# Optimization experiments

Measured on AMD Instinct MI355X. Metric: run time of the kernel, lower is better.

## Reference

```python
import jax, jax.numpy as jnp
import numpy as np

B, C, N = 2, 1024, 80
D = 3 * C + 2  # 3074 token dim
DFF = 2048     # torch TransformerEncoderLayer default dim_feedforward
HW = 224
REFINE = 3
EPS = 1e-5


def _layernorm(x, g, b):
    m = jnp.mean(x, axis=-1, keepdims=True)
    v = jnp.mean((x - m) ** 2, axis=-1, keepdims=True)
    return g * (x - m) / jnp.sqrt(v + EPS) + b


def _pos_encoding(seq_len, dim):
    pos = jnp.arange(seq_len, dtype=jnp.float32)[:, None]
    div = jnp.exp(jnp.arange(0, dim, 2, dtype=jnp.float32) * (-np.log(10000.0) / dim))
    pe = jnp.zeros((seq_len, dim), dtype=jnp.float32)
    pe = pe.at[:, 0::2].set(jnp.sin(pos * div)).at[:, 1::2].set(jnp.cos(pos * div))
    return pe


def _forward(pre_f, curr_f, first_f, ln_g, ln_b, ipw, ipb, opw, opb,
             n1g, n1b, l1w, l1b, l2w, l2b, n2g, n2b, ow, ob,
             prev_b, first_b):
    # --- vectorized find_best_shift: batched circular L1 correlation ---
    idx = (jnp.arange(N)[None, :] - jnp.arange(N)[:, None]) % N  # [shift, pos]
    rolled = first_b[:, idx]                                     # [B, N, N, 2]
    dist = jnp.abs(prev_b[:, None] - rolled).sum(axis=(-1, -2))  # [B, N]
    best = jnp.argmin(dist, axis=1)                              # first min, like torch loop
    roll_idx = (jnp.arange(N)[None, :] - best[:, None]) % N      # [B, N]
    first_b = jax.vmap(lambda fb, ri: fb[ri])(first_b, roll_idx)

    # --- bilinear upsample to 224x224 (F.interpolate, align_corners=False) ---
    up = lambda f: jax.image.resize(f, (f.shape[0], f.shape[1], HW, HW), method='bilinear')
    pre_up, curr_up, first_up = up(pre_f), up(curr_f), up(first_f)

    # --- vectorized get_bou_features: [B,N,C] gather ---
    gather = jax.vmap(lambda f, b: f[:, b[:, 0], b[:, 1]].T)
    pre_q = gather(pre_up, prev_b)      # [B, N, C]
    first_q = gather(first_up, first_b)  # [B, N, C]

    pe = _pos_encoding(N, D)
    curr = prev_b.astype(jnp.float32)
    scale = 1.0 / jnp.sqrt(jnp.float32(D))
    results = []
    for _ in range(REFINE):
        bf = gather(curr_up, curr.astype(jnp.int32))          # [B, N, C]
        tokens = jnp.concatenate([pre_q, bf, curr, first_q], axis=-1)  # [B, N, D]
        tokens = _layernorm(tokens, ln_g, ln_b)
        tokens = tokens + pe[None]
        # --- TransformerEncoderLayer (post-norm, nhead=1, relu, eval/no dropout) ---
        qkv = tokens @ ipw.T + ipb
        q, k, v = jnp.split(qkv, 3, axis=-1)
        attn = jax.nn.softmax(jnp.einsum('bqd,bkd->bqk', q, k) * scale, axis=-1)
        a = jnp.einsum('bqk,bkd->bqd', attn, v) @ opw.T + opb
        x = _layernorm(tokens + a, n1g, n1b)
        ff = jax.nn.relu(x @ l1w.T + l1b) @ l2w.T + l2b
        x = _layernorm(x + ff, n2g, n2b)
        out = x @ ow.T + ob                                   # [B, N, 1026]
        curr = jnp.clip(curr + out[..., C:], 0.0, 223.0)
        pre_q = pre_q + out[..., :C]
        results.append(curr)
    return jnp.stack(results)  # [REFINE, B, N, 2]


def setup_inputs() -> dict:
    key = jax.random.key(0)
    ks = jax.random.split(key, 12)
    f = lambda i, s: jax.random.normal(ks[i], s, dtype=jnp.float32)
    w = lambda i, s: 0.02 * jax.random.normal(ks[i], s, dtype=jnp.float32)
    return {
        'pre_img_features': f(0, (B, C, 14, 14)),
        'curr_img_features': f(1, (B, C, 14, 14)),
        'first_img_features': f(2, (B, C, 14, 14)),
        'previous_boundary': jax.random.randint(ks[3], (B, N, 2), 0, HW),
        'first_boundary': jax.random.randint(ks[4], (B, N, 2), 0, HW),
        'ln_g': jnp.ones((D,), jnp.float32), 'ln_b': jnp.zeros((D,), jnp.float32),
        'in_proj_w': w(5, (3 * D, D)), 'in_proj_b': jnp.zeros((3 * D,), jnp.float32),
        'out_proj_w': w(6, (D, D)), 'out_proj_b': jnp.zeros((D,), jnp.float32),
        'norm1_g': jnp.ones((D,), jnp.float32), 'norm1_b': jnp.zeros((D,), jnp.float32),
        'lin1_w': w(7, (DFF, D)), 'lin1_b': jnp.zeros((DFF,), jnp.float32),
        'lin2_w': w(8, (D, DFF)), 'lin2_b': jnp.zeros((D,), jnp.float32),
        'norm2_g': jnp.ones((D,), jnp.float32), 'norm2_b': jnp.zeros((D,), jnp.float32),
        'out_w': w(9, (C + 2, D)), 'out_b': jnp.zeros((C + 2,), jnp.float32),
    }


def reference(pre_img_features, curr_img_features, first_img_features,
              previous_boundary, first_boundary,
              ln_g, ln_b, in_proj_w, in_proj_b, out_proj_w, out_proj_b,
              norm1_g, norm1_b, lin1_w, lin1_b, lin2_w, lin2_b,
              norm2_g, norm2_b, out_w, out_b):
    return _forward(pre_img_features, curr_img_features, first_img_features,
                    ln_g, ln_b, in_proj_w, in_proj_b, out_proj_w, out_proj_b,
                    norm1_g, norm1_b, lin1_w, lin1_b, lin2_w, lin2_b,
                    norm2_g, norm2_b, out_w, out_b,
                    previous_boundary, first_boundary)
```

## Files before the change

kernel.cpp:

```cpp
#include <hip/hip_runtime.h>
#include <math.h>

#define B_    2
#define C_    1024
#define N_    80
#define D_    3074
#define DFF_  2048
#define OD_   1026
#define QKV_  9222
#define M_    160
#define EPS_  1e-5f
#define KPD_  3104

#define SQKV 6
#define SOP  14
#define SFF1 14
#define SFF2 16
#define SHD  14

typedef __attribute__((ext_vector_type(8))) short bf16x8;
typedef __attribute__((ext_vector_type(4))) float f32x4;

__device__ inline short f2bf(float f) {
    unsigned u = __float_as_uint(f);
    u += 0x7fffu + ((u >> 16) & 1u);
    return (short)(u >> 16);
}

__device__ inline float wave_sum(float v) {
#pragma unroll
    for (int off = 32; off > 0; off >>= 1) v += __shfl_down(v, off, 64);
    return v;
}

__device__ inline float wave_max(float v) {
#pragma unroll
    for (int off = 32; off > 0; off >>= 1) v = fmaxf(v, __shfl_down(v, off, 64));
    return v;
}

__device__ inline void block_reduce_2(float& s, float& s2, float* red) {
    int tid = threadIdx.x;
    int lane = tid & 63, wid = tid >> 6;
    s = wave_sum(s);
    s2 = wave_sum(s2);
    if (lane == 0) { red[wid] = s; red[4 + wid] = s2; }
    __syncthreads();
    if (tid == 0) {
        red[8] = red[0] + red[1] + red[2] + red[3];
        red[9] = red[4] + red[5] + red[6] + red[7];
    }
    __syncthreads();
    s = red[8]; s2 = red[9];
}

__device__ inline void bilin_setup(int p, int& i0, int& i1, float& t) {
    float s = (p + 0.5f) * 0.0625f - 0.5f;
    s = fminf(fmaxf(s, 0.0f), 13.0f);
    i0 = (int)s;
    t = s - (float)i0;
    i1 = min(i0 + 1, 13);
}

__device__ inline float bilin_tap(const float* f, int y0, int y1, float ty,
                                  int x0, int x1, float tx) {
    float a = f[y0 * 14 + x0], b = f[y0 * 14 + x1];
    float c = f[y1 * 14 + x0], d = f[y1 * 14 + x1];
    return (1.f - ty) * ((1.f - tx) * a + tx * b) + ty * ((1.f - tx) * c + tx * d);
}

__global__ __launch_bounds__(128) void align_kernel(const int* __restrict__ prev_b,
                                                    const int* __restrict__ first_b,
                                                    int* __restrict__ fb_al) {
    int b = blockIdx.x;
    int tid = threadIdx.x;
    __shared__ int dist[N_];
    __shared__ int bestIdx;
    if (tid < N_) {
        int s = 0;
        for (int j = 0; j < N_; ++j) {
            int src = (j - tid) % N_;
            if (src < 0) src += N_;
            int dy = prev_b[(b * N_ + j) * 2] - first_b[(b * N_ + src) * 2];
            int dx = prev_b[(b * N_ + j) * 2 + 1] - first_b[(b * N_ + src) * 2 + 1];
            s += abs(dy) + abs(dx);
        }
        dist[tid] = s;
    }
    __syncthreads();
    if (tid == 0) {
        int best = 0, bd = dist[0];
        for (int i = 1; i < N_; ++i)
            if (dist[i] < bd) { bd = dist[i]; best = i; }
        bestIdx = best;
    }
    __syncthreads();
    if (tid < N_) {
        int src = (tid - bestIdx) % N_;
        if (src < 0) src += N_;
        fb_al[(b * N_ + tid) * 2]     = first_b[(b * N_ + src) * 2];
        fb_al[(b * N_ + tid) * 2 + 1] = first_b[(b * N_ + src) * 2 + 1];
    }
}

__global__ __launch_bounds__(256) void gather_init_kernel(
        const float* __restrict__ pre_f, const float* __restrict__ first_f,
        const int* __restrict__ prev_b, const int* __restrict__ fb_al,
        float* __restrict__ pre_q, float* __restrict__ first_q,
        float* __restrict__ curr) {
    int m = blockIdx.x;
    int b = m / N_;
    int tid = threadIdx.x;
    int py = prev_b[m * 2], px = prev_b[m * 2 + 1];
    int fy = fb_al[m * 2], fx = fb_al[m * 2 + 1];
    int py0, py1, px0, px1, fy0, fy1, fx0, fx1;
    float pty, ptx, fty, ftx;
    bilin_setup(py, py0, py1, pty);
    bilin_setup(px, px0, px1, ptx);
    bilin_setup(fy, fy0, fy1, fty);
    bilin_setup(fx, fx0, fx1, ftx);
    for (int c = tid; c < C_; c += 256) {
        const float* fp = pre_f + (size_t)(b * C_ + c) * 196;
        const float* ff = first_f + (size_t)(b * C_ + c) * 196;
        pre_q[(size_t)m * C_ + c]   = bilin_tap(fp, py0, py1, pty, px0, px1, ptx);
        first_q[(size_t)m * C_ + c] = bilin_tap(ff, fy0, fy1, fty, fx0, fx1, ftx);
    }
    if (tid < 2) curr[m * 2 + tid] = (float)prev_b[m * 2 + tid];
}

__global__ __launch_bounds__(256) void tokens_kernel(
        const float* __restrict__ curr_f, const float* __restrict__ pre_q,
        const float* __restrict__ first_q, const float* __restrict__ curr,
        const float* __restrict__ ln_g, const float* __restrict__ ln_b,
        float* __restrict__ tokens, short* __restrict__ tokens_bf) {
    int m = blockIdx.x;
    int b = m / N_;
    int n = m % N_;
    int tid = threadIdx.x;
    __shared__ float bf[C_];
    __shared__ float red[10];

    float cy = curr[m * 2], cx = curr[m * 2 + 1];
    int iy = (int)cy, ix = (int)cx;
    int y0, y1, x0, x1;
    float ty, tx;
    bilin_setup(iy, y0, y1, ty);
    bilin_setup(ix, x0, x1, tx);
    for (int c = tid; c < C_; c += 256) {
        const float* f = curr_f + (size_t)(b * C_ + c) * 196;
        bf[c] = bilin_tap(f, y0, y1, ty, x0, x1, tx);
    }
    __syncthreads();

    float s = 0.f, s2 = 0.f;
    for (int d = tid; d < D_; d += 256) {
        float v;
        if (d < C_)            v = pre_q[(size_t)m * C_ + d];
        else if (d < 2 * C_)   v = bf[d - C_];
        else if (d == 2 * C_)  v = cy;
        else if (d == 2*C_+1)  v = cx;
        else                   v = first_q[(size_t)m * C_ + (d - 2 * C_ - 2)];
        s += v; s2 += v * v;
    }
    block_reduce_2(s, s2, red);
    float mean = s / (float)D_;
    float var = s2 / (float)D_ - mean * mean;
    float inv = rsqrtf(var + EPS_);

    const float negLogDivD = -logf(10000.0f) / (float)D_;
    for (int d = tid; d < KPD_; d += 256) {
        if (d < D_) {
            float v;
            if (d < C_)            v = pre_q[(size_t)m * C_ + d];
            else if (d < 2 * C_)   v = bf[d - C_];
            else if (d == 2 * C_)  v = cy;
            else if (d == 2*C_+1)  v = cx;
            else                   v = first_q[(size_t)m * C_ + (d - 2 * C_ - 2)];
            float ln = ln_g[d] * (v - mean) * inv + ln_b[d];
            int kk = d >> 1;
            float ang = (float)n * expf((float)(2 * kk) * negLogDivD);
            float pe = (d & 1) ? cosf(ang) : sinf(ang);
            float val = ln + pe;
            tokens[(size_t)m * D_ + d] = val;
            tokens_bf[(size_t)m * KPD_ + d] = f2bf(val);
        } else {
            tokens_bf[(size_t)m * KPD_ + d] = 0;
        }
    }
}

__global__ __launch_bounds__(256) void wpack_kernel(const float* __restrict__ w,
                                                    short* __restrict__ o,
                                                    int K, int O, int nch) {
    int s = blockIdx.x;
    int items = nch * 64;
    int qlen = (items + 3) >> 2;
    int beg = blockIdx.y * qlen;
    int end = min(items, beg + qlen);
    for (int idx = beg + threadIdx.x; idx < end; idx += 256) {
        int c = idx >> 6, l = idx & 63;
        int col = l & 15, quad = l >> 4;
        int orow = s * 16 + col;
        int k0 = c * 32 + quad * 8;
        bf16x8 v;
        if (orow < O && k0 + 8 <= K) {
            const float* src = w + (size_t)orow * K + k0;
            float2 a = *(const float2*)(src);
            float2 b = *(const float2*)(src + 2);
            float2 cc = *(const float2*)(src + 4);
            float2 d = *(const float2*)(src + 6);
            v[0] = f2bf(a.x);  v[1] = f2bf(a.y);
            v[2] = f2bf(b.x);  v[3] = f2bf(b.y);
            v[4] = f2bf(cc.x); v[5] = f2bf(cc.y);
            v[6] = f2bf(d.x);  v[7] = f2bf(d.y);
        } else {
#pragma unroll
            for (int j = 0; j < 8; ++j) {
                int k = k0 + j;
                v[j] = (orow < O && k < K) ? f2bf(w[(size_t)orow * K + k]) : (short)0;
            }
        }
        *(bf16x8*)(o + ((size_t)s * nch + c) * 512 + l * 8) = v;
    }
}

template <int SW>
__global__ __launch_bounds__(256) void gemm_stage(
        const short* __restrict__ A, const short* __restrict__ Wp,
        const float* __restrict__ bias, float* __restrict__ part,
        int KpA, int nch, int O, int per) {
    int cs = blockIdx.y * per;
    int ce = min(nch, cs + per);
    if (cs >= ce) return;
    int tid = threadIdx.x;
    int lane = tid & 63, wave = tid >> 6;
    int col = lane & 15, quad = lane >> 4;
    int s0 = (blockIdx.x * 4 + wave) * SW;

    __shared__ short lbuf[2][160 * 32];

    int m0 = tid >> 2, p8 = (tid & 3) * 8;
    int m1 = (tid + 256) >> 2;
    int m2 = (tid + 512) >> 2;
    const short* a0 = A + (size_t)m0 * KpA + p8;
    const short* a1 = A + (size_t)m1 * KpA + p8;
    const short* a2 = A + (size_t)m2 * KpA + p8;
    bf16x8 sr0, sr1, sr2;

    f32x4 acc[SW][10];
#pragma unroll
    for (int j = 0; j < SW; ++j)
#pragma unroll
        for (int t = 0; t < 10; ++t)
#pragma unroll
            for (int r = 0; r < 4; ++r) acc[j][t][r] = 0.f;

    const short* wbase[SW];
#pragma unroll
    for (int j = 0; j < SW; ++j)
        wbase[j] = Wp + (size_t)(s0 + j) * nch * 512 + lane * 8;
    bf16x8 wc[SW], wn[SW];

    sr0 = *(const bf16x8*)(a0 + cs * 32);
    sr1 = *(const bf16x8*)(a1 + cs * 32);
    if (tid < 128) sr2 = *(const bf16x8*)(a2 + cs * 32);
#pragma unroll
    for (int j = 0; j < SW; ++j)
        wc[j] = *(const bf16x8*)(wbase[j] + (size_t)cs * 512);
    *(bf16x8*)(&lbuf[0][m0 * 32 + p8]) = sr0;
    *(bf16x8*)(&lbuf[0][m1 * 32 + p8]) = sr1;
    if (tid < 128) *(bf16x8*)(&lbuf[0][m2 * 32 + p8]) = sr2;
    __syncthreads();

    int cur = 0;
    for (int c = cs; c < ce; ++c) {
        bool more = (c + 1) < ce;
        if (more) {
            sr0 = *(const bf16x8*)(a0 + (c + 1) * 32);
            sr1 = *(const bf16x8*)(a1 + (c + 1) * 32);
            if (tid < 128) sr2 = *(const bf16x8*)(a2 + (c + 1) * 32);
#pragma unroll
            for (int j = 0; j < SW; ++j)
                wn[j] = *(const bf16x8*)(wbase[j] + (size_t)(c + 1) * 512);
        }
#pragma unroll
        for (int t = 0; t < 10; ++t) {
            bf16x8 af = *(const bf16x8*)(&lbuf[cur][t * 512 + col * 32 + quad * 8]);
#pragma unroll
            for (int j = 0; j < SW; ++j)
                acc[j][t] = __builtin_amdgcn_mfma_f32_16x16x32_bf16(af, wc[j], acc[j][t], 0, 0, 0);
        }
        if (more) {
            *(bf16x8*)(&lbuf[cur ^ 1][m0 * 32 + p8]) = sr0;
            *(bf16x8*)(&lbuf[cur ^ 1][m1 * 32 + p8]) = sr1;
            if (tid < 128) *(bf16x8*)(&lbuf[cur ^ 1][m2 * 32 + p8]) = sr2;
        }
        __syncthreads();
#pragma unroll
        for (int j = 0; j < SW; ++j) wc[j] = wn[j];
        cur ^= 1;
    }

    float* pout = part + (size_t)blockIdx.y * M_ * O;
#pragma unroll
    for (int j = 0; j < SW; ++j) {
        int oc = (s0 + j) * 16 + col;
        if (oc < O) {
            float bv = (blockIdx.y == 0) ? bias[oc] : 0.f;
#pragma unroll
            for (int t = 0; t < 10; ++t)
#pragma unroll
                for (int r = 0; r < 4; ++r)
                    pout[(size_t)(t * 16 + quad * 4 + r) * O + oc] = acc[j][t][r] + bv;
        }
    }
}

__global__ __launch_bounds__(256) void gemm_pk(
        const short* __restrict__ A, const short* __restrict__ Wp,
        const float* __restrict__ bias, float* __restrict__ Cout,
        int KpA, int nch, int O) {
    int strip = blockIdx.x;
    int nsk = gridDim.y;
    int mg = blockIdx.z;
    int lane = threadIdx.x & 63, wave = threadIdx.x >> 6;
    int col = lane & 15, quad = lane >> 4;

    int per = (nch + nsk - 1) / nsk;
    int cs = blockIdx.y * per;
    int ce = min(nch, cs + per);
    if (cs >= ce) return;
    int tot = ce - cs;
    int qn = tot >> 2, rmd = tot & 3;
    int c0 = cs + wave * qn + min(wave, rmd);
    int c1 = c0 + qn + (wave < rmd ? 1 : 0);

    const short* wp = Wp + (size_t)strip * nch * 512 + lane * 8;
    const short* ap = A + (size_t)(mg * 80 + col) * KpA + quad * 8;

    f32x4 acc[5];
#pragma unroll
    for (int t = 0; t < 5; ++t)
#pragma unroll
        for (int r = 0; r < 4; ++r) acc[t][r] = 0.f;

    if (c0 < c1) {
        bf16x8 wcur = *(const bf16x8*)(wp + (size_t)c0 * 512);
        for (int c = c0; c < c1; ++c) {
            bf16x8 wnxt = wcur;
            if (c + 1 < c1) wnxt = *(const bf16x8*)(wp + (size_t)(c + 1) * 512);
#pragma unroll
            for (int t = 0; t < 5; ++t) {
                bf16x8 af = *(const bf16x8*)(ap + (size_t)t * 16 * KpA + c * 32);
                acc[t] = __builtin_amdgcn_mfma_f32_16x16x32_bf16(af, wcur, acc[t], 0, 0, 0);
            }
            wcur = wnxt;
        }
    }

    __shared__ f32x4 red[4][5][64];
#pragma unroll
    for (int t = 0; t < 5; ++t) red[wave][t][lane] = acc[t];
    __syncthreads();
    for (int item = threadIdx.x; item < 320; item += 256) {
        int t = item >> 6, l2 = item & 63;
        f32x4 v = red[0][t][l2];
#pragma unroll
        for (int w = 1; w < 4; ++w)
#pragma unroll
            for (int r = 0; r < 4; ++r) v[r] += red[w][t][l2][r];
        int oc = strip * 16 + (l2 & 15);
        if (oc < O) {
            float bv = (blockIdx.y == 0) ? bias[oc] : 0.f;
            int rbase = mg * 80 + t * 16 + (l2 >> 4) * 4;
#pragma unroll
            for (int r = 0; r < 4; ++r) {
                float val = v[r] + bv;
                if (nsk == 1) Cout[(size_t)(rbase + r) * O + oc] = val;
                else atomicAdd(&Cout[(size_t)(rbase + r) * O + oc], val);
            }
        }
    }
}

__global__ __launch_bounds__(256) void gemm_mfma_sk(
        const short* __restrict__ A, const float* __restrict__ Wf,
        const float* __restrict__ bias, float* __restrict__ Cout,
        int K, int KpA, int O, int KC) {
    int kc0 = blockIdx.y * KC;
    if (kc0 >= K) return;
    int kend = min(K, kc0 + KC);

    int lane = threadIdx.x & 63;
    int wave = threadIdx.x >> 6;
    int col  = lane & 15;
    int quad = lane >> 4;
    int o0 = blockIdx.x * 128 + wave * 32 + col;
    int o1 = o0 + 16;
    int oc0 = min(o0, O - 1), oc1 = min(o1, O - 1);

    const float* wrow0 = Wf + (size_t)oc0 * K + quad * 8;
    const float* wrow1 = Wf + (size_t)oc1 * K + quad * 8;
    const short* abase = A + (size_t)col * KpA + quad * 8;

    f32x4 acc0[10], acc1[10];
#pragma unroll
    for (int t = 0; t < 10; ++t)
#pragma unroll
        for (int r = 0; r < 4; ++r) { acc0[t][r] = 0.f; acc1[t][r] = 0.f; }

    int nfull = (kend - kc0) >> 5;
    bf16x8 aCur[10];
    float2 wCur[8];
    if (nfull > 0) {
#pragma unroll
        for (int t = 0; t < 10; ++t)
            aCur[t] = *(const bf16x8*)(abase + (size_t)t * 16 * KpA + kc0);
#pragma unroll
        for (int j = 0; j < 4; ++j) {
            wCur[j]     = *(const float2*)(wrow0 + kc0 + 2 * j);
            wCur[4 + j] = *(const float2*)(wrow1 + kc0 + 2 * j);
        }
    }
    for (int i = 0; i < nfull; ++i) {
        bf16x8 aNxt[10];
        float2 wNxt[8];
        if (i + 1 < nfull) {
            int kn = kc0 + (i + 1) * 32;
#pragma unroll
            for (int t = 0; t < 10; ++t)
                aNxt[t] = *(const bf16x8*)(abase + (size_t)t * 16 * KpA + kn);
#pragma unroll
            for (int j = 0; j < 4; ++j) {
                wNxt[j]     = *(const float2*)(wrow0 + kn + 2 * j);
                wNxt[4 + j] = *(const float2*)(wrow1 + kn + 2 * j);
            }
        }
        bf16x8 b0, b1;
#pragma unroll
        for (int j = 0; j < 4; ++j) {
            b0[2*j] = f2bf(wCur[j].x);     b0[2*j+1] = f2bf(wCur[j].y);
            b1[2*j] = f2bf(wCur[4+j].x);   b1[2*j+1] = f2bf(wCur[4+j].y);
        }
#pragma unroll
        for (int t = 0; t < 10; ++t) {
            acc0[t] = __builtin_amdgcn_mfma_f32_16x16x32_bf16(aCur[t], b0, acc0[t], 0, 0, 0);
            acc1[t] = __builtin_amdgcn_mfma_f32_16x16x32_bf16(aCur[t], b1, acc1[t], 0, 0, 0);
        }
#pragma unroll
        for (int t = 0; t < 10; ++t) aCur[t] = aNxt[t];
#pragma unroll
        for (int j = 0; j < 8; ++j) wCur[j] = wNxt[j];
    }
    int kmain = kc0 + nfull * 32;
    if (kmain < kend) {
        bf16x8 b0, b1;
#pragma unroll
        for (int j = 0; j < 8; ++j) {
            int k = kmain + quad * 8 + j;
            b0[j] = (k < kend) ? f2bf(Wf[(size_t)oc0 * K + k]) : (short)0;
            b1[j] = (k < kend) ? f2bf(Wf[(size_t)oc1 * K + k]) : (short)0;
        }
#pragma unroll
        for (int t = 0; t < 10; ++t) {
            bf16x8 af = *(const bf16x8*)(abase + (size_t)t * 16 * KpA + kmain);
            acc0[t] = __builtin_amdgcn_mfma_f32_16x16x32_bf16(af, b0, acc0[t], 0, 0, 0);
            acc1[t] = __builtin_amdgcn_mfma_f32_16x16x32_bf16(af, b1, acc1[t], 0, 0, 0);
        }
    }
    if (o0 < O) {
        float bv = (blockIdx.y == 0) ? bias[o0] : 0.f;
#pragma unroll
        for (int t = 0; t < 10; ++t)
#pragma unroll
            for (int r = 0; r < 4; ++r)
                atomicAdd(&Cout[(size_t)(t * 16 + quad * 4 + r) * O + o0], acc0[t][r] + bv);
    }
    if (o1 < O) {
        float bv = (blockIdx.y == 0) ? bias[o1] : 0.f;
#pragma unroll
        for (int t = 0; t < 10; ++t)
#pragma unroll
            for (int r = 0; r < 4; ++r)
                atomicAdd(&Cout[(size_t)(t * 16 + quad * 4 + r) * O + o1], acc1[t][r] + bv);
    }
}

__global__ __launch_bounds__(256) void relu_cvt_kernel(const float* __restrict__ in,
                                                       int S, size_t sstr,
                                                       short* __restrict__ out,
                                                       int n) {
    int i = blockIdx.x * 256 + threadIdx.x;
    if (i < n) {
        float v = 0.f;
        for (int s = 0; s < S; ++s) v += in[(size_t)s * sstr + i];
        out[i] = f2bf(fmaxf(v, 0.f));
    }
}

__global__ __launch_bounds__(256) void qkv_cvt_kernel(const float* __restrict__ part,
                                                      int S,
                                                      short* __restrict__ q_bf,
                                                      short* __restrict__ k_bf,
                                                      short* __restrict__ v_bf) {
    int m = blockIdx.x;
    int b = m / N_, q = m % N_;
    for (int d = threadIdx.x; d < KPD_; d += 256) {
        short qv = 0, kv = 0, vv = 0;
        if (d < D_) {
            float qf = 0.f, kf = 0.f, vf = 0.f;
            for (int s = 0; s < S; ++s) {
                const float* p = part + (size_t)s * M_ * QKV_ + (size_t)m * QKV_;
                qf += p[d]; kf += p[D_ + d]; vf += p[2 * D_ + d];
            }
            qv = f2bf(qf); kv = f2bf(kf); vv = f2bf(vf);
        }
        q_bf[(size_t)m * KPD_ + d] = qv;
        k_bf[(size_t)m * KPD_ + d] = kv;
        v_bf[((size_t)b * 96 + q) * KPD_ + d] = vv;
    }
}

__global__ __launch_bounds__(256) void scores_mfma(const short* __restrict__ q_bf,
                                                   const short* __restrict__ k_bf,
                                                   float* __restrict__ sc) {
    int bi = blockIdx.x;
    int b = bi / 25, qt = (bi % 25) / 5, kt = bi % 5;
    int lane = threadIdx.x & 63, wave = threadIdx.x >> 6;
    int col = lane & 15, quad = lane >> 4;
    const short* qbase = q_bf + (size_t)(b * N_ + qt * 16 + col) * KPD_ + quad * 8;
    const short* kbase = k_bf + (size_t)(b * N_ + kt * 16 + col) * KPD_ + quad * 8;
    f32x4 acc;
#pragma unroll
    for (int r = 0; r < 4; ++r) acc[r] = 0.f;
    int c0 = wave * 25, c1 = min(97, c0 + 25);
    for (int c = c0; c < c1; ++c) {
        bf16x8 af = *(const bf16x8*)(qbase + c * 32);
        bf16x8 bf8 = *(const bf16x8*)(kbase + c * 32);
        acc = __builtin_amdgcn_mfma_f32_16x16x32_bf16(af, bf8, acc, 0, 0, 0);
    }
    __shared__ f32x4 red[4][64];
    red[wave][lane] = acc;
    __syncthreads();
    if (threadIdx.x < 64) {
        f32x4 t = red[0][lane];
#pragma unroll
        for (int w = 1; w < 4; ++w)
#pragma unroll
            for (int r = 0; r < 4; ++r) t[r] += red[w][lane][r];
        float scale = rsqrtf((float)D_);
#pragma unroll
        for (int r = 0; r < 4; ++r)
            sc[(size_t)(b * N_ + qt * 16 + quad * 4 + r) * N_ + kt * 16 + col] = t[r] * scale;
    }
}

__global__ __launch_bounds__(256) void softmax_kernel(const float* __restrict__ sc,
                                                      short* __restrict__ p_bf) {
    int m = blockIdx.x * 4 + (threadIdx.x >> 6);
    int lane = threadIdx.x & 63;
    const float* row = sc + (size_t)m * N_;
    float a = row[lane];
    float bv = (lane < 16) ? row[64 + lane] : -1e30f;
    float mx = wave_max(fmaxf(a, bv));
    mx = __shfl(mx, 0, 64);
    float e0 = expf(a - mx);
    float e1 = (lane < 16) ? expf(bv - mx) : 0.f;
    float sum = wave_sum(e0 + e1);
    sum = __shfl(sum, 0, 64);
    float rs = 1.0f / sum;
    p_bf[(size_t)m * 96 + lane] = f2bf(e0 * rs);
    if (lane < 32)
        p_bf[(size_t)m * 96 + 64 + lane] = (lane < 16) ? f2bf(e1 * rs) : (short)0;
}

__global__ __launch_bounds__(256) void av_mfma(const short* __restrict__ p_bf,
                                               const short* __restrict__ v_bf,
                                               short* __restrict__ av_bf) {
    int bi = blockIdx.x;
    int b = bi / 49, g = bi % 49;
    int lane = threadIdx.x & 63, wave = threadIdx.x >> 6;
    int dtile = g * 4 + wave;
    if (dtile >= 194) return;
    int d0 = dtile * 16;
    int col = lane & 15, quad = lane >> 4;
    const short* pbase = p_bf + (size_t)b * N_ * 96 + quad * 8;
    const short* vb = v_bf + (size_t)b * 96 * KPD_ + d0 + col;
    f32x4 acc[5];
#pragma unroll
    for (int t = 0; t < 5; ++t)
#pragma unroll
        for (int r = 0; r < 4; ++r) acc[t][r] = 0.f;
#pragma unroll
    for (int c = 0; c < 3; ++c) {
        bf16x8 bf8;
#pragma unroll
        for (int j = 0; j < 8; ++j)
            bf8[j] = vb[(size_t)(c * 32 + quad * 8 + j) * KPD_];
#pragma unroll
        for (int t = 0; t < 5; ++t) {
            bf16x8 af = *(const bf16x8*)(pbase + (size_t)(t * 16 + col) * 96 + c * 32);
            acc[t] = __builtin_amdgcn_mfma_f32_16x16x32_bf16(af, bf8, acc[t], 0, 0, 0);
        }
    }
#pragma unroll
    for (int t = 0; t < 5; ++t)
#pragma unroll
        for (int r = 0; r < 4; ++r)
            av_bf[(size_t)(b * N_ + t * 16 + quad * 4 + r) * KPD_ + d0 + col] = f2bf(acc[t][r]);
}

template <bool WF32>
__global__ __launch_bounds__(256) void ln_kernel(const float* __restrict__ xin,
                                                 int S, size_t sstr,
                                                 const float* __restrict__ res,
                                                 const float* __restrict__ g,
                                                 const float* __restrict__ bta,
                                                 float* __restrict__ outf,
                                                 short* __restrict__ outb) {
    int m = blockIdx.x;
    int tid = threadIdx.x;
    __shared__ float red[10];
    const float* xr = xin + (size_t)m * D_;
    const float* rr = res + (size_t)m * D_;
    float vv[13];
    float s = 0.f, s2 = 0.f;
#pragma unroll
    for (int i = 0; i < 13; ++i) {
        int d = tid + i * 256;
        float v = 0.f;
        if (d < D_) {
            v = rr[d];
            for (int sp = 0; sp < S; ++sp) v += xr[(size_t)sp * sstr + d];
            s += v; s2 += v * v;
        }
        vv[i] = v;
    }
    block_reduce_2(s, s2, red);
    float mean = s / (float)D_;
    float var = s2 / (float)D_ - mean * mean;
    float inv = rsqrtf(var + EPS_);
#pragma unroll
    for (int i = 0; i < 13; ++i) {
        int d = tid + i * 256;
        if (d < D_) {
            float y = g[d] * (vv[i] - mean) * inv + bta[d];
            if (WF32) outf[(size_t)m * D_ + d] = y;
            outb[(size_t)m * KPD_ + d] = f2bf(y);
        } else if (d < KPD_) {
            outb[(size_t)m * KPD_ + d] = 0;
        }
    }
}

__global__ __launch_bounds__(256) void update_kernel(const float* __restrict__ part,
                                                     int S, size_t sstr,
                                                     float* __restrict__ curr,
                                                     float* __restrict__ pre_q,
                                                     float* __restrict__ results) {
    int m = blockIdx.x;
    int tid = threadIdx.x;
    const float* pr = part + (size_t)m * OD_;
    for (int c = tid; c < C_; c += 256) {
        float v = 0.f;
        for (int s = 0; s < S; ++s) v += pr[(size_t)s * sstr + c];
        pre_q[(size_t)m * C_ + c] += v;
    }
    if (tid < 2) {
        float v = 0.f;
        for (int s = 0; s < S; ++s) v += pr[(size_t)s * sstr + C_ + tid];
        float nc = curr[m * 2 + tid] + v;
        nc = fminf(fmaxf(nc, 0.f), 223.f);
        curr[m * 2 + tid] = nc;
        results[m * 2 + tid] = nc;
    }
}

extern "C" void kernel_launch(void* const* d_in, const int* in_sizes, int n_in,
                              void* d_out, int out_size, void* d_ws, size_t ws_size,
                              hipStream_t stream) {
    const float* pre_f   = (const float*)d_in[0];
    const float* curr_f  = (const float*)d_in[1];
    const float* first_f = (const float*)d_in[2];
    const int*   prev_b  = (const int*)d_in[3];
    const int*   first_b = (const int*)d_in[4];
    const float* ln_g    = (const float*)d_in[5];
    const float* ln_b    = (const float*)d_in[6];
    const float* ipw     = (const float*)d_in[7];
    const float* ipb     = (const float*)d_in[8];
    const float* opw     = (const float*)d_in[9];
    const float* opb     = (const float*)d_in[10];
    const float* n1g     = (const float*)d_in[11];
    const float* n1b     = (const float*)d_in[12];
    const float* l1w     = (const float*)d_in[13];
    const float* l1b     = (const float*)d_in[14];
    const float* l2w     = (const float*)d_in[15];
    const float* l2b     = (const float*)d_in[16];
    const float* n2g     = (const float*)d_in[17];
    const float* n2b     = (const float*)d_in[18];
    const float* ow      = (const float*)d_in[19];
    const float* ob      = (const float*)d_in[20];
    float* outp = (float*)d_out;

    float* wf = (float*)d_ws;
    size_t off = 0;
    int*   fb_al   = (int*)(wf + off); off += 320;
    float* curr    = wf + off;         off += 320;
    float* pre_q   = wf + off;         off += (size_t)M_ * C_;
    float* first_q = wf + off;         off += (size_t)M_ * C_;
    float* tokens  = wf + off;         off += (size_t)M_ * D_;
    float* xbuf    = wf + off;         off += (size_t)M_ * D_;
    float* sc      = wf + off;         off += (size_t)M_ * N_;
    short* tokens_bf = (short*)(wf + off); off += (size_t)M_ * KPD_ / 2;
    short* x_bf      = (short*)(wf + off); off += (size_t)M_ * KPD_ / 2;
    short* x2_bf     = (short*)(wf + off); off += (size_t)M_ * KPD_ / 2;
    short* av_bf     = (short*)(wf + off); off += (size_t)M_ * KPD_ / 2;
    short* ff1_bf    = (short*)(wf + off); off += (size_t)M_ * DFF_ / 2;
    short* q_bf      = (short*)(wf + off); off += (size_t)M_ * KPD_ / 2;
    short* k_bf      = (short*)(wf + off); off += (size_t)M_ * KPD_ / 2;
    short* v_bf      = (short*)(wf + off); off += (size_t)B_ * 96 * KPD_ / 2;
    short* p_bf      = (short*)(wf + off); off += (size_t)M_ * 96 / 2;
    size_t commonF = off;

    size_t o2 = commonF;
    short* ipw_p2 = (short*)(wf + o2); o2 += (size_t)584 * 97 * 256;
    short* opw_p2 = (short*)(wf + o2); o2 += (size_t)200 * 97 * 256;
    short* l1w_p2 = (short*)(wf + o2); o2 += (size_t)128 * 97 * 256;
    short* l2w_p2 = (short*)(wf + o2); o2 += (size_t)200 * 64 * 256;
    short* ow_p2  = (short*)(wf + o2); o2 += (size_t)68  * 97 * 256;
    float* gpart  = wf + o2;           o2 += (size_t)SQKV * M_ * QKV_;

    size_t o1 = commonF;
    float* qkv   = wf + o1; o1 += (size_t)M_ * QKV_;
    float* aout  = wf + o1; o1 += (size_t)M_ * D_;
    float* ff1f  = wf + o1; o1 += (size_t)M_ * DFF_;
    float* ffout = wf + o1; o1 += (size_t)M_ * D_;
    float* outb  = wf + o1; o1 += (size_t)M_ * OD_;
    size_t o0 = o1;
    short* ipw_p1 = (short*)(wf + o1); o1 += (size_t)577 * 97 * 256;
    short* opw_p1 = (short*)(wf + o1); o1 += (size_t)193 * 97 * 256;
    short* l1w_p1 = (short*)(wf + o1); o1 += (size_t)128 * 97 * 256;
    short* l2w_p1 = (short*)(wf + o1); o1 += (size_t)193 * 64 * 256;
    short* ow_p1  = (short*)(wf + o1); o1 += (size_t)65  * 97 * 256;

    int tier = (ws_size >= o2 * sizeof(float)) ? 2
             : (ws_size >= o1 * sizeof(float)) ? 1
             : 0;
    (void)in_sizes; (void)n_in; (void)out_size; (void)o0;

    hipLaunchKernelGGL(align_kernel, dim3(B_), dim3(128), 0, stream,
                       prev_b, first_b, fb_al);
    hipLaunchKernelGGL(gather_init_kernel, dim3(M_), dim3(256), 0, stream,
                       pre_f, first_f, prev_b, fb_al, pre_q, first_q, curr);
    hipMemsetAsync(v_bf, 0, (size_t)B_ * 96 * KPD_ * 2, stream);

    if (tier == 2) {
        hipLaunchKernelGGL(wpack_kernel, dim3(584, 4), dim3(256), 0, stream, ipw, ipw_p2, D_, QKV_, 97);
        hipLaunchKernelGGL(wpack_kernel, dim3(200, 4), dim3(256), 0, stream, opw, opw_p2, D_, D_, 97);
        hipLaunchKernelGGL(wpack_kernel, dim3(128, 4), dim3(256), 0, stream, l1w, l1w_p2, D_, DFF_, 97);
        hipLaunchKernelGGL(wpack_kernel, dim3(200, 4), dim3(256), 0, stream, l2w, l2w_p2, DFF_, D_, 64);
        hipLaunchKernelGGL(wpack_kernel, dim3(68, 4),  dim3(256), 0, stream, ow, ow_p2, D_, OD_, 97);
    } else if (tier == 1) {
        hipLaunchKernelGGL(wpack_kernel, dim3(577, 4), dim3(256), 0, stream, ipw, ipw_p1, D_, QKV_, 97);
        hipLaunchKernelGGL(wpack_kernel, dim3(193, 4), dim3(256), 0, stream, opw, opw_p1, D_, D_, 97);
        hipLaunchKernelGGL(wpack_kernel, dim3(128, 4), dim3(256), 0, stream, l1w, l1w_p1, D_, DFF_, 97);
        hipLaunchKernelGGL(wpack_kernel, dim3(193, 4), dim3(256), 0, stream, l2w, l2w_p1, DFF_, D_, 64);
        hipLaunchKernelGGL(wpack_kernel, dim3(65, 4),  dim3(256), 0, stream, ow, ow_p1, D_, OD_, 97);
    }

    for (int it = 0; it < 3; ++it) {
        if (tier < 2) {
            if (tier == 0) hipMemsetAsync(qkv, 0, (size_t)M_ * QKV_ * 4, stream);
            hipMemsetAsync(aout,  0, (size_t)M_ * D_   * 4, stream);
            hipMemsetAsync(ff1f,  0, (size_t)M_ * DFF_ * 4, stream);
            hipMemsetAsync(ffout, 0, (size_t)M_ * D_   * 4, stream);
            hipMemsetAsync(outb,  0, (size_t)M_ * OD_  * 4, stream);
        }

        hipLaunchKernelGGL(tokens_kernel, dim3(M_), dim3(256), 0, stream,
                           curr_f, pre_q, first_q, curr, ln_g, ln_b, tokens, tokens_bf);
        if (tier == 2)
            hipLaunchKernelGGL((gemm_stage<2>), dim3(73, SQKV), dim3(256), 0, stream,
                               tokens_bf, ipw_p2, ipb, gpart, KPD_, 97, QKV_, (97 + SQKV - 1) / SQKV);
        else if (tier == 1)
            hipLaunchKernelGGL(gemm_pk, dim3(577, 1, 2), dim3(256), 0, stream,
                               tokens_bf, ipw_p1, ipb, qkv, KPD_, 97, QKV_);
        else
            hipLaunchKernelGGL(gemm_mfma_sk, dim3(73, 6), dim3(256), 0, stream,
                               tokens_bf, ipw, ipb, qkv, D_, KPD_, QKV_, 544);
        hipLaunchKernelGGL(qkv_cvt_kernel, dim3(M_), dim3(256), 0, stream,
                           (tier == 2) ? gpart : qkv, (tier == 2) ? SQKV : 1,
                           q_bf, k_bf, v_bf);
        hipLaunchKernelGGL(scores_mfma, dim3(50), dim3(256), 0, stream,
                           q_bf, k_bf, sc);
        hipLaunchKernelGGL(softmax_kernel, dim3(40), dim3(256), 0, stream,
                           sc, p_bf);
        hipLaunchKernelGGL(av_mfma, dim3(98), dim3(256), 0, stream,
                           p_bf, v_bf, av_bf);
        if (tier == 2)
            hipLaunchKernelGGL((gemm_stage<2>), dim3(25, SOP), dim3(256), 0, stream,
                               av_bf, opw_p2, opb, gpart, KPD_, 97, D_, (97 + SOP - 1) / SOP);
        else if (tier == 1)
            hipLaunchKernelGGL(gemm_pk, dim3(193, 2, 2), dim3(256), 0, stream,
                               av_bf, opw_p1, opb, aout, KPD_, 97, D_);
        else
            hipLaunchKernelGGL(gemm_mfma_sk, dim3(25, 10), dim3(256), 0, stream,
                               av_bf, opw, opb, aout, D_, KPD_, D_, 320);
        hipLaunchKernelGGL((ln_kernel<true>), dim3(M_), dim3(256), 0, stream,
                           (tier == 2) ? gpart : aout, (tier == 2) ? SOP : 1, (size_t)M_ * D_,
                           tokens, n1g, n1b, xbuf, x_bf);
        if (tier == 2)
            hipLaunchKernelGGL((gemm_stage<2>), dim3(16, SFF1), dim3(256), 0, stream,
                               x_bf, l1w_p2, l1b, gpart, KPD_, 97, DFF_, (97 + SFF1 - 1) / SFF1);
        else if (tier == 1)
            hipLaunchKernelGGL(gemm_pk, dim3(128, 2, 2), dim3(256), 0, stream,
                               x_bf, l1w_p1, l1b, ff1f, KPD_, 97, DFF_);
        else
            hipLaunchKernelGGL(gemm_mfma_sk, dim3(16, 17), dim3(256), 0, stream,
                               x_bf, l1w, l1b, ff1f, D_, KPD_, DFF_, 192);
        hipLaunchKernelGGL(relu_cvt_kernel, dim3((M_ * DFF_ + 255) / 256), dim3(256), 0, stream,
                           (tier == 2) ? gpart : ff1f, (tier == 2) ? SFF1 : 1, (size_t)M_ * DFF_,
                           ff1_bf, M_ * DFF_);
        if (tier == 2)
            hipLaunchKernelGGL((gemm_stage<2>), dim3(25, SFF2), dim3(256), 0, stream,
                               ff1_bf, l2w_p2, l2b, gpart, DFF_, 64, D_, (64 + SFF2 - 1) / SFF2);
        else if (tier == 1)
            hipLaunchKernelGGL(gemm_pk, dim3(193, 2, 2), dim3(256), 0, stream,
                               ff1_bf, l2w_p1, l2b, ffout, DFF_, 64, D_);
        else
            hipLaunchKernelGGL(gemm_mfma_sk, dim3(25, 11), dim3(256), 0, stream,
                               ff1_bf, l2w, l2b, ffout, DFF_, DFF_, D_, 192);
        hipLaunchKernelGGL((ln_kernel<false>), dim3(M_), dim3(256), 0, stream,
                           (tier == 2) ? gpart : ffout, (tier == 2) ? SFF2 : 1, (size_t)M_ * D_,
                           xbuf, n2g, n2b, (float*)nullptr, x2_bf);
        if (tier == 2)
            hipLaunchKernelGGL((gemm_stage<1>), dim3(17, SHD), dim3(256), 0, stream,
                               x2_bf, ow_p2, ob, gpart, KPD_, 97, OD_, (97 + SHD - 1) / SHD);
        else if (tier == 1)
            hipLaunchKernelGGL(gemm_pk, dim3(65, 4, 2), dim3(256), 0, stream,
                               x2_bf, ow_p1, ob, outb, KPD_, 97, OD_);
        else
            hipLaunchKernelGGL(gemm_mfma_sk, dim3(9, 13), dim3(256), 0, stream,
                               x2_bf, ow, ob, outb, D_, KPD_, OD_, 256);
        hipLaunchKernelGGL(update_kernel, dim3(M_), dim3(256), 0, stream,
                           (tier == 2) ? gpart : outb, (tier == 2) ? SHD : 1, (size_t)M_ * OD_,
                           curr, pre_q, outp + (size_t)it * M_ * 2);
    }
}
```

Measured before the change: 1.134 ms.

## Widen split-K GEMM blocks to 8 waves, cut split count, precompute PE, LDS-stage weight pack

The split-K GEMM stage now runs 512-thread blocks with 8 waves sharing each staged activation tile, and every projection uses a fixed split of 4 instead of 6–16. This cuts the partial-sum buffers that the downstream conversion and layernorm kernels must reduce, at the cost of fewer blocks in flight. Positional encodings are computed once into a table instead of recomputing exp/sin/cos in every token pass. The weight-pack kernel now stages rows through LDS for coalesced reads, and the unused middle fallback tier is removed.

```diff
diff --git a/kernel.cpp b/kernel.cpp
--- a/kernel.cpp
+++ b/kernel.cpp
@@ -11,12 +11,7 @@
 #define M_    160
 #define EPS_  1e-5f
 #define KPD_  3104
-
-#define SQKV 6
-#define SOP  14
-#define SFF1 14
-#define SFF2 16
-#define SHD  14
+#define SPL_  4
 
 typedef __attribute__((ext_vector_type(8))) short bf16x8;
 typedef __attribute__((ext_vector_type(4))) float f32x4;
@@ -128,10 +123,21 @@
     if (tid < 2) curr[m * 2 + tid] = (float)prev_b[m * 2 + tid];
 }
 
+__global__ __launch_bounds__(256) void pe_kernel(float* __restrict__ pe) {
+    int n = blockIdx.x;
+    const float negLogDivD = -logf(10000.0f) / (float)D_;
+    for (int d = threadIdx.x; d < D_; d += 256) {
+        int kk = d >> 1;
+        float ang = (float)n * expf((float)(2 * kk) * negLogDivD);
+        pe[(size_t)n * D_ + d] = (d & 1) ? cosf(ang) : sinf(ang);
+    }
+}
+
 __global__ __launch_bounds__(256) void tokens_kernel(
         const float* __restrict__ curr_f, const float* __restrict__ pre_q,
         const float* __restrict__ first_q, const float* __restrict__ curr,
         const float* __restrict__ ln_g, const float* __restrict__ ln_b,
+        const float* __restrict__ pe_tab,
         float* __restrict__ tokens, short* __restrict__ tokens_bf) {
     int m = blockIdx.x;
     int b = m / N_;
@@ -167,7 +173,6 @@
     float var = s2 / (float)D_ - mean * mean;
     float inv = rsqrtf(var + EPS_);
 
-    const float negLogDivD = -logf(10000.0f) / (float)D_;
     for (int d = tid; d < KPD_; d += 256) {
         if (d < D_) {
             float v;
@@ -177,10 +182,7 @@
             else if (d == 2*C_+1)  v = cx;
             else                   v = first_q[(size_t)m * C_ + (d - 2 * C_ - 2)];
             float ln = ln_g[d] * (v - mean) * inv + ln_b[d];
-            int kk = d >> 1;
-            float ang = (float)n * expf((float)(2 * kk) * negLogDivD);
-            float pe = (d & 1) ? cosf(ang) : sinf(ang);
-            float val = ln + pe;
+            float val = ln + pe_tab[(size_t)n * D_ + d];
             tokens[(size_t)m * D_ + d] = val;
             tokens_bf[(size_t)m * KPD_ + d] = f2bf(val);
         } else {
@@ -189,43 +191,46 @@
     }
 }
 
+#define WPK_CH 25
 __global__ __launch_bounds__(256) void wpack_kernel(const float* __restrict__ w,
                                                     short* __restrict__ o,
                                                     int K, int O, int nch) {
     int s = blockIdx.x;
-    int items = nch * 64;
-    int qlen = (items + 3) >> 2;
-    int beg = blockIdx.y * qlen;
-    int end = min(items, beg + qlen);
-    for (int idx = beg + threadIdx.x; idx < end; idx += 256) {
-        int c = idx >> 6, l = idx & 63;
+    int nq = (nch + 3) >> 2;
+    int c0 = blockIdx.y * nq;
+    int c1 = min(nch, c0 + nq);
+    int ncq = c1 - c0;
+    if (ncq <= 0) return;
+    __shared__ short lds[16][WPK_CH * 32 + 8];
+
+    int kbase = c0 * 32;
+    int ktot = ncq * 32;
+    int npair = ktot >> 1;
+    for (int idx = threadIdx.x; idx < 16 * npair; idx += 256) {
+        int r = idx / npair;
+        int kp = idx % npair;
+        int orow = s * 16 + r;
+        int k = kbase + kp * 2;
+        float2 v = make_float2(0.f, 0.f);
+        if (orow < O && k + 1 < K)
+            v = *(const float2*)(w + (size_t)orow * K + k);
+        lds[r][kp * 2]     = f2bf(v.x);
+        lds[r][kp * 2 + 1] = f2bf(v.y);
+    }
+    __syncthreads();
+    for (int idx = threadIdx.x; idx < ncq * 64; idx += 256) {
+        int ci = idx >> 6, l = idx & 63;
         int col = l & 15, quad = l >> 4;
-        int orow = s * 16 + col;
-        int k0 = c * 32 + quad * 8;
         bf16x8 v;
-        if (orow < O && k0 + 8 <= K) {
-            const float* src = w + (size_t)orow * K + k0;
-            float2 a = *(const float2*)(src);
-            float2 b = *(const float2*)(src + 2);
-            float2 cc = *(const float2*)(src + 4);
-            float2 d = *(const float2*)(src + 6);
-            v[0] = f2bf(a.x);  v[1] = f2bf(a.y);
-            v[2] = f2bf(b.x);  v[3] = f2bf(b.y);
-            v[4] = f2bf(cc.x); v[5] = f2bf(cc.y);
-            v[6] = f2bf(d.x);  v[7] = f2bf(d.y);
-        } else {
-#pragma unroll
-            for (int j = 0; j < 8; ++j) {
-                int k = k0 + j;
-                v[j] = (orow < O && k < K) ? f2bf(w[(size_t)orow * K + k]) : (short)0;
-            }
-        }
-        *(bf16x8*)(o + ((size_t)s * nch + c) * 512 + l * 8) = v;
+#pragma unroll
+        for (int j = 0; j < 8; ++j)
+            v[j] = lds[col][ci * 32 + quad * 8 + j];
+        *(bf16x8*)(o + ((size_t)s * nch + (c0 + ci)) * 512 + (size_t)l * 8) = v;
     }
 }
 
 template <int SW>
-__global__ __launch_bounds__(256) void gemm_stage(
+__global__ __launch_bounds__(512) void gemm_stage(
         const short* __restrict__ A, const short* __restrict__ Wp,
         const float* __restrict__ bias, float* __restrict__ part,
         int KpA, int nch, int O, int per) {
@@ -235,17 +240,15 @@
     int tid = threadIdx.x;
     int lane = tid & 63, wave = tid >> 6;
     int col = lane & 15, quad = lane >> 4;
-    int s0 = (blockIdx.x * 4 + wave) * SW;
+    int s0 = (blockIdx.x * 8 + wave) * SW;
 
     __shared__ short lbuf[2][160 * 32];
 
     int m0 = tid >> 2, p8 = (tid & 3) * 8;
-    int m1 = (tid + 256) >> 2;
-    int m2 = (tid + 512) >> 2;
+    int m1 = (tid + 512) >> 2;
     const short* a0 = A + (size_t)m0 * KpA + p8;
     const short* a1 = A + (size_t)m1 * KpA + p8;
-    const short* a2 = A + (size_t)m2 * KpA + p8;
-    bf16x8 sr0, sr1, sr2;
+    bf16x8 sr0, sr1;
 
     f32x4 acc[SW][10];
 #pragma unroll
@@ -258,27 +261,24 @@
     const short* wbase[SW];
 #pragma unroll
     for (int j = 0; j < SW; ++j)
-        wbase[j] = Wp + (size_t)(s0 + j) * nch * 512 + lane * 8;
+        wbase[j] = Wp + (size_t)(s0 + j) * nch * 512 + (size_t)lane * 8;
     bf16x8 wc[SW], wn[SW];
 
-    sr0 = *(const bf16x8*)(a0 + cs * 32);
-    sr1 = *(const bf16x8*)(a1 + cs * 32);
-    if (tid < 128) sr2 = *(const bf16x8*)(a2 + cs * 32);
+    sr0 = *(const bf16x8*)(a0 + (size_t)cs * 32);
+    if (tid < 128) sr1 = *(const bf16x8*)(a1 + (size_t)cs * 32);
 #pragma unroll
     for (int j = 0; j < SW; ++j)
         wc[j] = *(const bf16x8*)(wbase[j] + (size_t)cs * 512);
     *(bf16x8*)(&lbuf[0][m0 * 32 + p8]) = sr0;
-    *(bf16x8*)(&lbuf[0][m1 * 32 + p8]) = sr1;
-    if (tid < 128) *(bf16x8*)(&lbuf[0][m2 * 32 + p8]) = sr2;
+    if (tid < 128) *(bf16x8*)(&lbuf[0][m1 * 32 + p8]) = sr1;
     __syncthreads();
 
     int cur = 0;
     for (int c = cs; c < ce; ++c) {
         bool more = (c + 1) < ce;
         if (more) {
-            sr0 = *(const bf16x8*)(a0 + (c + 1) * 32);
-            sr1 = *(const bf16x8*)(a1 + (c + 1) * 32);
-            if (tid < 128) sr2 = *(const bf16x8*)(a2 + (c + 1) * 32);
+            sr0 = *(const bf16x8*)(a0 + (size_t)(c + 1) * 32);
+            if (tid < 128) sr1 = *(const bf16x8*)(a1 + (size_t)(c + 1) * 32);
 #pragma unroll
             for (int j = 0; j < SW; ++j)
                 wn[j] = *(const bf16x8*)(wbase[j] + (size_t)(c + 1) * 512);
@@ -292,8 +292,7 @@
         }
         if (more) {
             *(bf16x8*)(&lbuf[cur ^ 1][m0 * 32 + p8]) = sr0;
-            *(bf16x8*)(&lbuf[cur ^ 1][m1 * 32 + p8]) = sr1;
-            if (tid < 128) *(bf16x8*)(&lbuf[cur ^ 1][m2 * 32 + p8]) = sr2;
+            if (tid < 128) *(bf16x8*)(&lbuf[cur ^ 1][m1 * 32 + p8]) = sr1;
         }
         __syncthreads();
 #pragma unroll
@@ -312,73 +311,6 @@
 #pragma unroll
                 for (int r = 0; r < 4; ++r)
                     pout[(size_t)(t * 16 + quad * 4 + r) * O + oc] = acc[j][t][r] + bv;
-        }
-    }
-}
-
-__global__ __launch_bounds__(256) void gemm_pk(
-        const short* __restrict__ A, const short* __restrict__ Wp,
-        const float* __restrict__ bias, float* __restrict__ Cout,
-        int KpA, int nch, int O) {
-    int strip = blockIdx.x;
-    int nsk = gridDim.y;
-    int mg = blockIdx.z;
-    int lane = threadIdx.x & 63, wave = threadIdx.x >> 6;
-    int col = lane & 15, quad = lane >> 4;
-
-    int per = (nch + nsk - 1) / nsk;
-    int cs = blockIdx.y * per;
-    int ce = min(nch, cs + per);
-    if (cs >= ce) return;
-    int tot = ce - cs;
-    int qn = tot >> 2, rmd = tot & 3;
-    int c0 = cs + wave * qn + min(wave, rmd);
-    int c1 = c0 + qn + (wave < rmd ? 1 : 0);
-
-    const short* wp = Wp + (size_t)strip * nch * 512 + lane * 8;
-    const short* ap = A + (size_t)(mg * 80 + col) * KpA + quad * 8;
-
-    f32x4 acc[5];
-#pragma unroll
-    for (int t = 0; t < 5; ++t)
-#pragma unroll
-        for (int r = 0; r < 4; ++r) acc[t][r] = 0.f;
-
-    if (c0 < c1) {
-        bf16x8 wcur = *(const bf16x8*)(wp + (size_t)c0 * 512);
-        for (int c = c0; c < c1; ++c) {
-            bf16x8 wnxt = wcur;
-            if (c + 1 < c1) wnxt = *(const bf16x8*)(wp + (size_t)(c + 1) * 512);
-#pragma unroll
-            for (int t = 0; t < 5; ++t) {
-                bf16x8 af = *(const bf16x8*)(ap + (size_t)t * 16 * KpA + c * 32);
-                acc[t] = __builtin_amdgcn_mfma_f32_16x16x32_bf16(af, wcur, acc[t], 0, 0, 0);
-            }
-            wcur = wnxt;
-        }
-    }
-
-    __shared__ f32x4 red[4][5][64];
-#pragma unroll
-    for (int t = 0; t < 5; ++t) red[wave][t][lane] = acc[t];
-    __syncthreads();
-    for (int item = threadIdx.x; item < 320; item += 256) {
-        int t = item >> 6, l2 = item & 63;
-        f32x4 v = red[0][t][l2];
-#pragma unroll
-        for (int w = 1; w < 4; ++w)
-#pragma unroll
-            for (int r = 0; r < 4; ++r) v[r] += red[w][t][l2][r];
-        int oc = strip * 16 + (l2 & 15);
-        if (oc < O) {
-            float bv = (blockIdx.y == 0) ? bias[oc] : 0.f;
-            int rbase = mg * 80 + t * 16 + (l2 >> 4) * 4;
-#pragma unroll
-            for (int r = 0; r < 4; ++r) {
-                float val = v[r] + bv;
-                if (nsk == 1) Cout[(size_t)(rbase + r) * O + oc] = val;
-                else atomicAdd(&Cout[(size_t)(rbase + r) * O + oc], val);
-            }
         }
     }
 }
@@ -711,6 +643,7 @@
     float* tokens  = wf + off;         off += (size_t)M_ * D_;
     float* xbuf    = wf + off;         off += (size_t)M_ * D_;
     float* sc      = wf + off;         off += (size_t)M_ * N_;
+    float* pe_tab  = wf + off;         off += (size_t)N_ * D_;
     short* tokens_bf = (short*)(wf + off); off += (size_t)M_ * KPD_ / 2;
     short* x_bf      = (short*)(wf + off); off += (size_t)M_ * KPD_ / 2;
     short* x2_bf     = (short*)(wf + off); off += (size_t)M_ * KPD_ / 2;
@@ -723,54 +656,41 @@
     size_t commonF = off;
 
     size_t o2 = commonF;
-    short* ipw_p2 = (short*)(wf + o2); o2 += (size_t)584 * 97 * 256;
-    short* opw_p2 = (short*)(wf + o2); o2 += (size_t)200 * 97 * 256;
+    short* ipw_p2 = (short*)(wf + o2); o2 += (size_t)592 * 97 * 256;
+    short* opw_p2 = (short*)(wf + o2); o2 += (size_t)208 * 97 * 256;
     short* l1w_p2 = (short*)(wf + o2); o2 += (size_t)128 * 97 * 256;
-    short* l2w_p2 = (short*)(wf + o2); o2 += (size_t)200 * 64 * 256;
-    short* ow_p2  = (short*)(wf + o2); o2 += (size_t)68  * 97 * 256;
-    float* gpart  = wf + o2;           o2 += (size_t)SQKV * M_ * QKV_;
-
-    size_t o1 = commonF;
-    float* qkv   = wf + o1; o1 += (size_t)M_ * QKV_;
-    float* aout  = wf + o1; o1 += (size_t)M_ * D_;
-    float* ff1f  = wf + o1; o1 += (size_t)M_ * DFF_;
-    float* ffout = wf + o1; o1 += (size_t)M_ * D_;
-    float* outb  = wf + o1; o1 += (size_t)M_ * OD_;
-    size_t o0 = o1;
-    short* ipw_p1 = (short*)(wf + o1); o1 += (size_t)577 * 97 * 256;
-    short* opw_p1 = (short*)(wf + o1); o1 += (size_t)193 * 97 * 256;
-    short* l1w_p1 = (short*)(wf + o1); o1 += (size_t)128 * 97 * 256;
-    short* l2w_p1 = (short*)(wf + o1); o1 += (size_t)193 * 64 * 256;
-    short* ow_p1  = (short*)(wf + o1); o1 += (size_t)65  * 97 * 256;
-
-    int tier = (ws_size >= o2 * sizeof(float)) ? 2
-             : (ws_size >= o1 * sizeof(float)) ? 1
-             : 0;
-    (void)in_sizes; (void)n_in; (void)out_size; (void)o0;
+    short* l2w_p2 = (short*)(wf + o2); o2 += (size_t)208 * 64 * 256;
+    short* ow_p2  = (short*)(wf + o2); o2 += (size_t)80  * 97 * 256;
+    float* gpart  = wf + o2;           o2 += (size_t)SPL_ * M_ * QKV_;
+
+    size_t o0 = commonF;
+    float* qkv   = wf + o0; o0 += (size_t)M_ * QKV_;
+    float* aout  = wf + o0; o0 += (size_t)M_ * D_;
+    float* ff1f  = wf + o0; o0 += (size_t)M_ * DFF_;
+    float* ffout = wf + o0; o0 += (size_t)M_ * D_;
+    float* outb  = wf + o0; o0 += (size_t)M_ * OD_;
+
+    int tier = (ws_size >= o2 * sizeof(float)) ? 2 : 0;
+    (void)in_sizes; (void)n_in; (void)out_size;
 
     hipLaunchKernelGGL(align_kernel, dim3(B_), dim3(128), 0, stream,
                        prev_b, first_b, fb_al);
     hipLaunchKernelGGL(gather_init_kernel, dim3(M_), dim3(256), 0, stream,
                        pre_f, first_f, prev_b, fb_al, pre_q, first_q, curr);
+    hipLaunchKernelGGL(pe_kernel, dim3(N_), dim3(256), 0, stream, pe_tab);
     hipMemsetAsync(v_bf, 0, (size_t)B_ * 96 * KPD_ * 2, stream);
 
     if (tier == 2) {
-        hipLaunchKernelGGL(wpack_kernel, dim3(584, 4), dim3(256), 0, stream, ipw, ipw_p2, D_, QKV_, 97);
-        hipLaunchKernelGGL(wpack_kernel, dim3(200, 4), dim3(256), 0, stream, opw, opw_p2, D_, D_, 97);
+        hipLaunchKernelGGL(wpack_kernel, dim3(592, 4), dim3(256), 0, stream, ipw, ipw_p2, D_, QKV_, 97);
+        hipLaunchKernelGGL(wpack_kernel, dim3(208, 4), dim3(256), 0, stream, opw, opw_p2, D_, D_, 97);
         hipLaunchKernelGGL(wpack_kernel, dim3(128, 4), dim3(256), 0, stream, l1w, l1w_p2, D_, DFF_, 97);
-        hipLaunchKernelGGL(wpack_kernel, dim3(200, 4), dim3(256), 0, stream, l2w, l2w_p2, DFF_, D_, 64);
-        hipLaunchKernelGGL(wpack_kernel, dim3(68, 4),  dim3(256), 0, stream, ow, ow_p2, D_, OD_, 97);
-    } else if (tier == 1) {
-        hipLaunchKernelGGL(wpack_kernel, dim3(577, 4), dim3(256), 0, stream, ipw, ipw_p1, D_, QKV_, 97);
-        hipLaunchKernelGGL(wpack_kernel, dim3(193, 4), dim3(256), 0, stream, opw, opw_p1, D_, D_, 97);
-        hipLaunchKernelGGL(wpack_kernel, dim3(128, 4), dim3(256), 0, stream, l1w, l1w_p1, D_, DFF_, 97);
-        hipLaunchKernelGGL(wpack_kernel, dim3(193, 4), dim3(256), 0, stream, l2w, l2w_p1, DFF_, D_, 64);
-        hipLaunchKernelGGL(wpack_kernel, dim3(65, 4),  dim3(256), 0, stream, ow, ow_p1, D_, OD_, 97);
+        hipLaunchKernelGGL(wpack_kernel, dim3(208, 4), dim3(256), 0, stream, l2w, l2w_p2, DFF_, D_, 64);
+        hipLaunchKernelGGL(wpack_kernel, dim3(80, 4),  dim3(256), 0, stream, ow, ow_p2, D_, OD_, 97);
     }
 
     for (int it = 0; it < 3; ++it) {
-        if (tier < 2) {
-            if (tier == 0) hipMemsetAsync(qkv, 0, (size_t)M_ * QKV_ * 4, stream);
+        if (tier == 0) {
+            hipMemsetAsync(qkv,   0, (size_t)M_ * QKV_ * 4, stream);
             hipMemsetAsync(aout,  0, (size_t)M_ * D_   * 4, stream);
             hipMemsetAsync(ff1f,  0, (size_t)M_ * DFF_ * 4, stream);
             hipMemsetAsync(ffout, 0, (size_t)M_ * D_   * 4, stream);
@@ -778,18 +698,16 @@
         }
 
         hipLaunchKernelGGL(tokens_kernel, dim3(M_), dim3(256), 0, stream,
-                           curr_f, pre_q, first_q, curr, ln_g, ln_b, tokens, tokens_bf);
+                           curr_f, pre_q, first_q, curr, ln_g, ln_b, pe_tab,
+                           tokens, tokens_bf);
         if (tier == 2)
-            hipLaunchKernelGGL((gemm_stage<2>), dim3(73, SQKV), dim3(256), 0, stream,
-                               tokens_bf, ipw_p2, ipb, gpart, KPD_, 97, QKV_, (97 + SQKV - 1) / SQKV);
-        else if (tier == 1)
-            hipLaunchKernelGGL(gemm_pk, dim3(577, 1, 2), dim3(256), 0, stream,
-                               tokens_bf, ipw_p1, ipb, qkv, KPD_, 97, QKV_);
+            hipLaunchKernelGGL((gemm_stage<2>), dim3(37, SPL_), dim3(512), 0, stream,
+                               tokens_bf, ipw_p2, ipb, gpart, KPD_, 97, QKV_, 25);
         else
             hipLaunchKernelGGL(gemm_mfma_sk, dim3(73, 6), dim3(256), 0, stream,
                                tokens_bf, ipw, ipb, qkv, D_, KPD_, QKV_, 544);
         hipLaunchKernelGGL(qkv_cvt_kernel, dim3(M_), dim3(256), 0, stream,
-                           (tier == 2) ? gpart : qkv, (tier == 2) ? SQKV : 1,
+                           (tier == 2) ? gpart : qkv, (tier == 2) ? SPL_ : 1,
                            q_bf, k_bf, v_bf);
         hipLaunchKernelGGL(scores_mfma, dim3(50), dim3(256), 0, stream,
                            q_bf, k_bf, sc);
@@ -798,52 +716,40 @@
         hipLaunchKernelGGL(av_mfma, dim3(98), dim3(256), 0, stream,
                            p_bf, v_bf, av_bf);
         if (tier == 2)
-            hipLaunchKernelGGL((gemm_stage<2>), dim3(25, SOP), dim3(256), 0, stream,
-                               av_bf, opw_p2, opb, gpart, KPD_, 97, D_, (97 + SOP - 1) / SOP);
-        else if (tier == 1)
-            hipLaunchKernelGGL(gemm_pk, dim3(193, 2, 2), dim3(256), 0, stream,
-                               av_bf, opw_p1, opb, aout, KPD_, 97, D_);
+            hipLaunchKernelGGL((gemm_stage<2>), dim3(13, SPL_), dim3(512), 0, stream,
+                               av_bf, opw_p2, opb, gpart, KPD_, 97, D_, 25);
         else
             hipLaunchKernelGGL(gemm_mfma_sk, dim3(25, 10), dim3(256), 0, stream,
                                av_bf, opw, opb, aout, D_, KPD_, D_, 320);
         hipLaunchKernelGGL((ln_kernel<true>), dim3(M_), dim3(256), 0, stream,
-                           (tier == 2) ? gpart : aout, (tier == 2) ? SOP : 1, (size_t)M_ * D_,
+                           (tier == 2) ? gpart : aout, (tier == 2) ? SPL_ : 1, (size_t)M_ * D_,
                            tokens, n1g, n1b, xbuf, x_bf);
         if (tier == 2)
-            hipLaunchKernelGGL((gemm_stage<2>), dim3(16, SFF1), dim3(256), 0, stream,
-                               x_bf, l1w_p2, l1b, gpart, KPD_, 97, DFF_, (97 + SFF1 - 1) / SFF1);
-        else if (tier == 1)
-            hipLaunchKernelGGL(gemm_pk, dim3(128, 2, 2), dim3(256), 0, stream,
-                               x_bf, l1w_p1, l1b, ff1f, KPD_, 97, DFF_);
+            hipLaunchKernelGGL((gemm_stage<2>), dim3(8, SPL_), dim3(512), 0, stream,
+                               x_bf, l1w_p2, l1b, gpart, KPD_, 97, DFF_, 25);
         else
             hipLaunchKernelGGL(gemm_mfma_sk, dim3(16, 17), dim3(256), 0, stream,
                                x_bf, l1w, l1b, ff1f, D_, KPD_, DFF_, 192);
         hipLaunchKernelGGL(relu_cvt_kernel, dim3((M_ * DFF_ + 255) / 256), dim3(256), 0, stream,
-                           (tier == 2) ? gpart : ff1f, (tier == 2) ? SFF1 : 1, (size_t)M_ * DFF_,
+                           (tier == 2) ? gpart : ff1f, (tier == 2) ? SPL_ : 1, (size_t)M_ * DFF_,
                            ff1_bf, M_ * DFF_);
         if (tier == 2)
-            hipLaunchKernelGGL((gemm_stage<2>), dim3(25, SFF2), dim3(256), 0, stream,
-                               ff1_bf, l2w_p2, l2b, gpart, DFF_, 64, D_, (64 + SFF2 - 1) / SFF2);
-        else if (tier == 1)
-            hipLaunchKernelGGL(gemm_pk, dim3(193, 2, 2), dim3(256), 0, stream,
-                               ff1_bf, l2w_p1, l2b, ffout, DFF_, 64, D_);
+            hipLaunchKernelGGL((gemm_stage<2>), dim3(13, SPL_), dim3(512), 0, stream,
+                               ff1_bf, l2w_p2, l2b, gpart, DFF_, 64, D_, 16);
         else
             hipLaunchKernelGGL(gemm_mfma_sk, dim3(25, 11), dim3(256), 0, stream,
                                ff1_bf, l2w, l2b, ffout, DFF_, DFF_, D_, 192);
         hipLaunchKernelGGL((ln_kernel<false>), dim3(M_), dim3(256), 0, stream,
-                           (tier == 2) ? gpart : ffout, (tier == 2) ? SFF2 : 1, (size_t)M_ * D_,
+                           (tier == 2) ? gpart : ffout, (tier == 2) ? SPL_ : 1, (size_t)M_ * D_,
                            xbuf, n2g, n2b, (float*)nullptr, x2_bf);
         if (tier == 2)
-            hipLaunchKernelGGL((gemm_stage<1>), dim3(17, SHD), dim3(256), 0, stream,
-                               x2_bf, ow_p2, ob, gpart, KPD_, 97, OD_, (97 + SHD - 1) / SHD);
-        else if (tier == 1)
-            hipLaunchKernelGGL(gemm_pk, dim3(65, 4, 2), dim3(256), 0, stream,
-                               x2_bf, ow_p1, ob, outb, KPD_, 97, OD_);
+            hipLaunchKernelGGL((gemm_stage<2>), dim3(5, SPL_), dim3(512), 0, stream,
+                               x2_bf, ow_p2, ob, gpart, KPD_, 97, OD_, 25);
         else
             hipLaunchKernelGGL(gemm_mfma_sk, dim3(9, 13), dim3(256), 0, stream,
                                x2_bf, ow, ob, outb, D_, KPD_, OD_, 256);
         hipLaunchKernelGGL(update_kernel, dim3(M_), dim3(256), 0, stream,
-                           (tier == 2) ? gpart : outb, (tier == 2) ? SHD : 1, (size_t)M_ * OD_,
+                           (tier == 2) ? gpart : outb, (tier == 2) ? SPL_ : 1, (size_t)M_ * OD_,
                            curr, pre_q, outp + (size_t)it * M_ * 2);
     }
 }
```

After: 1.090 ms. -3.8%, faster.
